# Kernel tuning notes

Measured on AMD Instinct MI355X. Metric: run time of the kernel, lower is better.

## Reference

```python
import jax, jax.numpy as jnp
import numpy as np

D, H, DH, FF, E, DHID, V, NL = 768, 12, 64, 3072, 8, 2048, 50258, 6
CAP, THRESH = 256, 0.2  # capacity = int(512 * 2.0 * 2 / 8), threshold_eval


def _ln(x, g, b):
    m = jnp.mean(x, -1, keepdims=True)
    v = jnp.mean(jnp.square(x - m), -1, keepdims=True)
    return (x - m) * jax.lax.rsqrt(v + 1e-5) * g + b


def _rms(x, g):
    return x * jax.lax.rsqrt(jnp.mean(jnp.square(x), -1, keepdims=True) + 1e-6) * g


def _attn(x, wqkv, bqkv, wo, bo):
    b, s, _ = x.shape
    q, k, v = jnp.split(x @ wqkv + bqkv, 3, axis=-1)
    q, k, v = (t.reshape(b, s, H, DH).transpose(0, 2, 1, 3) for t in (q, k, v))
    sc = jnp.einsum('bhqd,bhkd->bhqk', q, k) / 8.0  # sqrt(DH) = 8
    causal = jnp.tril(jnp.ones((s, s), bool))
    p = jax.nn.softmax(jnp.where(causal, sc, -1e9), axis=-1)
    o = jnp.einsum('bhqk,bhkd->bhqd', p, v).transpose(0, 2, 1, 3).reshape(b, s, D)
    return o @ wo + bo


def _mlp(x, w1, b1, w2, b2):  # GPT2 gelu_new = tanh approx
    return jax.nn.gelu(x @ w1 + b1, approximate=True) @ w2 + b2


def _geglu_ff(x, w1, b1, w2, b2):  # st-moe Expert FF
    a, g = jnp.split(x @ w1 + b1, 2, axis=-1)
    return (a * jax.nn.gelu(g, approximate=False)) @ w2 + b2


def _moe(x, wg, we1, be1, we2, be2):
    # top-2 gating with eval threshold + capacity-factor dispatch (ST-MoE style)
    logits = x @ wg                              # [b,s,E]
    probs = jax.nn.softmax(logits, axis=-1)
    idx1 = jnp.argmax(probs, -1)
    m1 = jax.nn.one_hot(idx1, E, dtype=x.dtype)
    gate1 = jnp.sum(probs * m1, -1)
    probs2 = probs * (1.0 - m1)
    idx2 = jnp.argmax(probs2, -1)
    m2r = jax.nn.one_hot(idx2, E, dtype=x.dtype)
    gate2 = jnp.sum(probs2 * m2r, -1)
    denom = gate1 + gate2 + 1e-9
    g1 = gate1 / denom
    keep_second = (gate2 > THRESH).astype(x.dtype)
    g2 = (gate2 / denom) * keep_second
    m2 = m2r * keep_second[..., None]
    # aux losses
    density = jnp.mean(m1, (0, 1))
    proxy = jnp.mean(probs, (0, 1))
    balance = jnp.mean(density * proxy) * (E * E)
    zloss = jnp.mean(jnp.square(jax.nn.logsumexp(logits, -1)))
    aux = 0.01 * balance + 0.001 * zloss
    # capacity positions (per batch group, first choices placed before second)
    pos1 = jnp.cumsum(m1, 1) - 1.0
    keep1 = m1 * (pos1 < CAP)
    cnt1 = jnp.sum(m1, 1, keepdims=True)
    pos2 = jnp.cumsum(m2, 1) - 1.0 + cnt1
    keep2 = m2 * (pos2 < CAP)
    oh1 = jax.nn.one_hot(pos1.astype(jnp.int32), CAP, dtype=x.dtype)
    oh2 = jax.nn.one_hot(pos2.astype(jnp.int32), CAP, dtype=x.dtype)
    combine = (g1[..., None, None] * keep1[..., None] * oh1
               + g2[..., None, None] * keep2[..., None] * oh2)  # [b,s,E,CAP]
    dispatch = (combine > 0).astype(x.dtype)
    xin = jnp.einsum('bsec,bsd->ebcd', dispatch, x)              # [E,b,CAP,D]
    h = jnp.einsum('ebcd,edf->ebcf', xin, we1) + be1[:, None, None, :]
    a, g = jnp.split(h, 2, axis=-1)
    h = a * jax.nn.gelu(g, approximate=False)
    out = jnp.einsum('ebcf,efd->ebcd', h, we2) + be2[:, None, None, :]
    y = jnp.einsum('bsec,ebcd->bsd', combine, out)
    return y, aux


def _moe_block(x, ffb_g, ffb_w1, ffb_b1, ffb_w2, ffb_b2, moe_g, w_gate,
               we1, be1, we2, be2, ffa_g, ffa_w1, ffa_b1, ffa_w2, ffa_b2):
    x = x + _geglu_ff(_rms(x, ffb_g), ffb_w1, ffb_b1, ffb_w2, ffb_b2)
    y, aux = _moe(_rms(x, moe_g), w_gate, we1, be1, we2, be2)
    x = x + y
    x = x + _geglu_ff(_rms(x, ffa_g), ffa_w1, ffa_b1, ffa_w2, ffa_b2)
    return x, aux


def _forward(input_ids, wte, wpe, ln1_g, ln1_b, w_qkv, b_qkv, w_ao, b_ao,
             ln2_g, ln2_b, w_fc, b_fc, w_mp, b_mp, lnf_g, lnf_b,
             ffb_g, ffb_w1, ffb_b1, ffb_w2, ffb_b2, moe_g, w_gate,
             we1, be1, we2, be2, ffa_g, ffa_w1, ffa_b1, ffa_w2, ffa_b2):
    s = input_ids.shape[1]
    x = wte[input_ids] + wpe[:s][None]
    aux_total = jnp.float32(0.0)
    moe_params = (ffb_g, ffb_w1, ffb_b1, ffb_w2, ffb_b2, moe_g, w_gate,
                  we1, be1, we2, be2, ffa_g, ffa_w1, ffa_b1, ffa_w2, ffa_b2)
    for i in range(NL):
        x = x + _attn(_ln(x, ln1_g[i], ln1_b[i]), w_qkv[i], b_qkv[i], w_ao[i], b_ao[i])
        h = _ln(x, ln2_g[i], ln2_b[i])
        if i in (0, 3):  # MoE layers (mlp*0 in source is a no-op)
            ff, aux = _moe_block(h, *moe_params)
            aux_total = aux_total + aux
            x = x + ff
        else:
            x = x + _mlp(h, w_fc[i], b_fc[i], w_mp[i], b_mp[i])
    x = _ln(x, lnf_g, lnf_b)
    return x @ wte.T, aux_total  # lm_head tied to wte


def setup_inputs() -> dict:
    key = jax.random.key(0)
    ks = iter(jax.random.split(key, 40))
    def nrm(shape):
        return (jax.random.normal(next(ks), shape) * 0.02).astype(jnp.float32)
    f32 = jnp.float32
    return {
        'input_ids': jax.random.randint(next(ks), (4, 512), 0, V),
        'attention_mask': jnp.ones((4, 512), jnp.int32),  # unused by the source forward
        'wte': nrm((V, D)), 'wpe': nrm((1024, D)),
        'ln1_g': jnp.ones((NL, D), f32), 'ln1_b': jnp.zeros((NL, D), f32),
        'w_qkv': nrm((NL, D, 3 * D)), 'b_qkv': jnp.zeros((NL, 3 * D), f32),
        'w_ao': nrm((NL, D, D)), 'b_ao': jnp.zeros((NL, D), f32),
        'ln2_g': jnp.ones((NL, D), f32), 'ln2_b': jnp.zeros((NL, D), f32),
        'w_fc': nrm((NL, D, FF)), 'b_fc': jnp.zeros((NL, FF), f32),
        'w_mp': nrm((NL, FF, D)), 'b_mp': jnp.zeros((NL, D), f32),
        'lnf_g': jnp.ones((D,), f32), 'lnf_b': jnp.zeros((D,), f32),
        'ffb_g': jnp.ones((D,), f32), 'ffb_w1': nrm((D, 2 * DHID)), 'ffb_b1': jnp.zeros((2 * DHID,), f32),
        'ffb_w2': nrm((DHID, D)), 'ffb_b2': jnp.zeros((D,), f32),
        'moe_g': jnp.ones((D,), f32), 'w_gate': nrm((D, E)),
        'we1': nrm((E, D, 2 * DHID)), 'be1': jnp.zeros((E, 2 * DHID), f32),
        'we2': nrm((E, DHID, D)), 'be2': jnp.zeros((E, D), f32),
        'ffa_g': jnp.ones((D,), f32), 'ffa_w1': nrm((D, 2 * DHID)), 'ffa_b1': jnp.zeros((2 * DHID,), f32),
        'ffa_w2': nrm((DHID, D)), 'ffa_b2': jnp.zeros((D,), f32),
    }


def reference(input_ids, attention_mask, wte, wpe, ln1_g, ln1_b, w_qkv, b_qkv,
              w_ao, b_ao, ln2_g, ln2_b, w_fc, b_fc, w_mp, b_mp, lnf_g, lnf_b,
              ffb_g, ffb_w1, ffb_b1, ffb_w2, ffb_b2, moe_g, w_gate,
              we1, be1, we2, be2, ffa_g, ffa_w1, ffa_b1, ffa_w2, ffa_b2):
    del attention_mask  # computed but never used in the source forward
    return _forward(input_ids, wte, wpe, ln1_g, ln1_b, w_qkv, b_qkv, w_ao, b_ao,
                    ln2_g, ln2_b, w_fc, b_fc, w_mp, b_mp, lnf_g, lnf_b,
                    ffb_g, ffb_w1, ffb_b1, ffb_w2, ffb_b2, moe_g, w_gate,
                    we1, be1, we2, be2, ffa_g, ffa_w1, ffa_b1, ffa_w2, ffa_b2)
```

## Files before the change

### kernel.cpp

```cpp
#include <hip/hip_runtime.h>
#include <math.h>

#define B_ 4
#define S_ 512
#define T_ 2048
#define D_ 768
#define H_ 12
#define DH_ 64
#define FF_ 3072
#define G_ 4096
#define DHID_ 2048
#define E_ 8
#define CAP_ 256
#define V_ 50258
#define NL_ 6

__device__ __forceinline__ float gelu_tanh_f(float x) {
    float x3 = x * x * x;
    return 0.5f * x * (1.0f + tanhf(0.7978845608028654f * (x + 0.044715f * x3)));
}
__device__ __forceinline__ float gelu_exact_f(float x) {
    return 0.5f * x * (1.0f + erff(x * 0.7071067811865475f));
}

__global__ __launch_bounds__(256) void embed_kernel(
    const int* __restrict__ ids, const float* __restrict__ wte,
    const float* __restrict__ wpe, float* __restrict__ x) {
    int t = blockIdx.x;
    int id = ids[t];
    int s = t & (S_ - 1);
    const float* wt = wte + (long long)id * D_;
    const float* wp = wpe + (long long)s * D_;
    float* o = x + (long long)t * D_;
    for (int c = threadIdx.x; c < D_; c += 256) o[c] = wt[c] + wp[c];
}

__global__ __launch_bounds__(256) void ln_kernel(
    const float* __restrict__ X, const float* __restrict__ g,
    const float* __restrict__ bb, float* __restrict__ out) {
    __shared__ float red[256];
    int t = blockIdx.x, tid = threadIdx.x;
    const float* x = X + (long long)t * D_;
    float v0 = x[tid], v1 = x[tid + 256], v2 = x[tid + 512];
    red[tid] = v0 + v1 + v2;
    __syncthreads();
    for (int o = 128; o; o >>= 1) { if (tid < o) red[tid] += red[tid + o]; __syncthreads(); }
    float mean = red[0] * (1.0f / D_);
    __syncthreads();
    float d0 = v0 - mean, d1 = v1 - mean, d2 = v2 - mean;
    red[tid] = d0 * d0 + d1 * d1 + d2 * d2;
    __syncthreads();
    for (int o = 128; o; o >>= 1) { if (tid < o) red[tid] += red[tid + o]; __syncthreads(); }
    float r = rsqrtf(red[0] * (1.0f / D_) + 1e-5f);
    float* op = out + (long long)t * D_;
    op[tid]       = d0 * r * g[tid]       + bb[tid];
    op[tid + 256] = d1 * r * g[tid + 256] + bb[tid + 256];
    op[tid + 512] = d2 * r * g[tid + 512] + bb[tid + 512];
}

__global__ __launch_bounds__(256) void rms_kernel(
    const float* __restrict__ X, const float* __restrict__ g, float* __restrict__ out) {
    __shared__ float red[256];
    int t = blockIdx.x, tid = threadIdx.x;
    const float* x = X + (long long)t * D_;
    float v0 = x[tid], v1 = x[tid + 256], v2 = x[tid + 512];
    red[tid] = v0 * v0 + v1 * v1 + v2 * v2;
    __syncthreads();
    for (int o = 128; o; o >>= 1) { if (tid < o) red[tid] += red[tid + o]; __syncthreads(); }
    float r = rsqrtf(red[0] * (1.0f / D_) + 1e-6f);
    float* op = out + (long long)t * D_;
    op[tid]       = v0 * r * g[tid];
    op[tid + 256] = v1 * r * g[tid + 256];
    op[tid + 512] = v2 * r * g[tid + 512];
}

template <int ACT, bool BIAS, bool RESID, bool BT>
__global__ __launch_bounds__(256) void gemm_kernel(
    const float* __restrict__ A, int lda, long long sA,
    const float* __restrict__ Bm, int ldb, long long sB,
    const float* __restrict__ bias, long long sBias,
    const float* __restrict__ Res,
    float* __restrict__ C, int ldc, long long sC,
    int M, int N, int K) {
    const int bz = blockIdx.z;
    const float* Ap = A + (long long)bz * sA;
    const float* Bp = Bm + (long long)bz * sB;
    const float* biasp = BIAS ? bias + (long long)bz * sBias : nullptr;
    const float* Resp = RESID ? Res + (long long)bz * sC : nullptr;
    float* Cp = C + (long long)bz * sC;

    const int m0 = blockIdx.y * 64;
    const int n0 = blockIdx.x * 64;
    const int tid = threadIdx.x;
    const int tx = tid & 15, ty = tid >> 4;

    __shared__ float As[16][65];
    __shared__ float Bs[16][65];

    float acc[4][4] = {};

    for (int k0 = 0; k0 < K; k0 += 16) {
        {
            int m = tid >> 2, kg = (tid & 3) * 4;
            float4 av = *(const float4*)(Ap + (long long)(m0 + m) * lda + k0 + kg);
            As[kg + 0][m] = av.x; As[kg + 1][m] = av.y;
            As[kg + 2][m] = av.z; As[kg + 3][m] = av.w;
        }
        if (!BT) {
            int k = tid >> 4, ng = (tid & 15) * 4;
            float4 bv = *(const float4*)(Bp + (long long)(k0 + k) * ldb + n0 + ng);
            Bs[k][ng + 0] = bv.x; Bs[k][ng + 1] = bv.y;
            Bs[k][ng + 2] = bv.z; Bs[k][ng + 3] = bv.w;
        } else {
            int n = tid >> 2, kg = (tid & 3) * 4;
            float4 bv = make_float4(0.f, 0.f, 0.f, 0.f);
            if (n0 + n < N)
                bv = *(const float4*)(Bp + (long long)(n0 + n) * ldb + k0 + kg);
            Bs[kg + 0][n] = bv.x; Bs[kg + 1][n] = bv.y;
            Bs[kg + 2][n] = bv.z; Bs[kg + 3][n] = bv.w;
        }
        __syncthreads();
#pragma unroll
        for (int k = 0; k < 16; ++k) {
            float a[4], b[4];
#pragma unroll
            for (int j = 0; j < 4; ++j) a[j] = As[k][ty * 4 + j];
#pragma unroll
            for (int j = 0; j < 4; ++j) b[j] = Bs[k][tx * 4 + j];
#pragma unroll
            for (int i = 0; i < 4; ++i)
#pragma unroll
                for (int j = 0; j < 4; ++j) acc[i][j] += a[i] * b[j];
        }
        __syncthreads();
    }

#pragma unroll
    for (int i = 0; i < 4; ++i) {
        int m = m0 + ty * 4 + i;
#pragma unroll
        for (int j = 0; j < 4; ++j) {
            int n = n0 + tx * 4 + j;
            if (n < N) {
                float v = acc[i][j];
                if (BIAS) v += biasp[n];
                if (ACT == 1) v = gelu_tanh_f(v);
                if (RESID) v += Resp[(long long)m * ldc + n];
                Cp[(long long)m * ldc + n] = v;
            }
        }
    }
}

template <int ACT, bool BIAS, bool RESID, bool BT>
static void launch_gemm(hipStream_t st, const float* A, int lda, long long sA,
                        const float* Bm, int ldb, long long sB,
                        const float* bias, long long sBias, const float* Res,
                        float* C, int ldc, long long sC, int M, int N, int K, int Z) {
    dim3 g((N + 63) / 64, M / 64, Z);
    gemm_kernel<ACT, BIAS, RESID, BT><<<g, 256, 0, st>>>(
        A, lda, sA, Bm, ldb, sB, bias, sBias, Res, C, ldc, sC, M, N, K);
}

__global__ __launch_bounds__(256) void attn_scores_kernel(
    const float* __restrict__ qkv, float* __restrict__ P) {
    int q = blockIdx.x, h = blockIdx.y, b = blockIdx.z;
    int tid = threadIdx.x;
    __shared__ float4 qv[16];
    __shared__ float red[256];
    const float* qrow = qkv + ((long long)(b * S_ + q)) * (3 * D_) + h * DH_;
    if (tid < 16) qv[tid] = *(const float4*)(qrow + tid * 4);
    __syncthreads();
    float sc[2];
#pragma unroll
    for (int r = 0; r < 2; ++r) {
        int k = tid + r * 256;
        float s = -1e30f;
        if (k <= q) {
            const float* krow = qkv + ((long long)(b * S_ + k)) * (3 * D_) + D_ + h * DH_;
            float dot = 0.f;
#pragma unroll
            for (int i = 0; i < 16; ++i) {
                float4 kv = *(const float4*)(krow + i * 4);
                float4 qq = qv[i];
                dot += qq.x * kv.x + qq.y * kv.y + qq.z * kv.z + qq.w * kv.w;
            }
            s = dot * 0.125f;
        }
        sc[r] = s;
    }
    float mx = fmaxf(sc[0], sc[1]);
    red[tid] = mx; __syncthreads();
    for (int o = 128; o; o >>= 1) { if (tid < o) red[tid] = fmaxf(red[tid], red[tid + o]); __syncthreads(); }
    mx = red[0]; __syncthreads();
    float e0 = (sc[0] > -1e29f) ? expf(sc[0] - mx) : 0.f;
    float e1 = (sc[1] > -1e29f) ? expf(sc[1] - mx) : 0.f;
    red[tid] = e0 + e1; __syncthreads();
    for (int o = 128; o; o >>= 1) { if (tid < o) red[tid] += red[tid + o]; __syncthreads(); }
    float inv = 1.0f / red[0];
    float* pr = P + (((long long)(b * H_ + h) * S_) + q) * S_;
    pr[tid] = e0 * inv;
    pr[tid + 256] = e1 * inv;
}

__global__ __launch_bounds__(64) void attn_pv_kernel(
    const float* __restrict__ qkv, const float* __restrict__ P, float* __restrict__ O) {
    int q = blockIdx.x, h = blockIdx.y, b = blockIdx.z;
    int d = threadIdx.x;
    const float* pr = P + (((long long)(b * H_ + h) * S_) + q) * S_;
    const float* vb = qkv + (long long)b * S_ * (3 * D_) + 2 * D_ + h * DH_ + d;
    float acc = 0.f;
    for (int k = 0; k <= q; ++k) acc += pr[k] * vb[(long long)k * (3 * D_)];
    O[((long long)(b * S_ + q)) * D_ + h * DH_ + d] = acc;
}

__global__ __launch_bounds__(256) void glu_kernel(
    const float* __restrict__ hb, float* __restrict__ ob, long long rows) {
    long long i = (long long)blockIdx.x * 256 + threadIdx.x;
    long long r = i >> 11;
    int c = (int)(i & (DHID_ - 1));
    float a = hb[r * G_ + c];
    float g = hb[r * G_ + DHID_ + c];
    ob[i] = a * gelu_exact_f(g);
}

__global__ __launch_bounds__(256) void moe_gate_kernel(
    const float* __restrict__ t0, const float* __restrict__ wg,
    int* __restrict__ idx1, int* __restrict__ idx2,
    float* __restrict__ g1o, float* __restrict__ g2o, float* __restrict__ red) {
    __shared__ float sred[17];
    int tid = threadIdx.x;
    if (tid < 17) sred[tid] = 0.f;
    __syncthreads();
    int t = blockIdx.x * 256 + tid;
    const float* xr = t0 + (long long)t * D_;
    float lg[E_];
#pragma unroll
    for (int e = 0; e < E_; ++e) lg[e] = 0.f;
    for (int i = 0; i < D_; ++i) {
        float xv = xr[i];
        const float* w = wg + i * E_;
#pragma unroll
        for (int e = 0; e < E_; ++e) lg[e] += xv * w[e];
    }
    float mx = lg[0];
#pragma unroll
    for (int e = 1; e < E_; ++e) mx = fmaxf(mx, lg[e]);
    float pe[E_], sum = 0.f;
#pragma unroll
    for (int e = 0; e < E_; ++e) { pe[e] = expf(lg[e] - mx); sum += pe[e]; }
    float lse = mx + logf(sum);
    float inv = 1.0f / sum;
#pragma unroll
    for (int e = 0; e < E_; ++e) pe[e] *= inv;
    int i1 = 0; float p1 = pe[0];
#pragma unroll
    for (int e = 1; e < E_; ++e) if (pe[e] > p1) { p1 = pe[e]; i1 = e; }
    int i2 = 0; float p2 = -1.f;
#pragma unroll
    for (int e = 0; e < E_; ++e) if (e != i1 && pe[e] > p2) { p2 = pe[e]; i2 = e; }
    float denom = p1 + p2 + 1e-9f;
    float g1 = p1 / denom;
    float keep = (p2 > 0.2f) ? 1.f : 0.f;
    float g2 = (p2 / denom) * keep;
    idx1[t] = i1; idx2[t] = i2; g1o[t] = g1; g2o[t] = g2;
    atomicAdd(&sred[i1], 1.0f);
#pragma unroll
    for (int e = 0; e < E_; ++e) atomicAdd(&sred[8 + e], pe[e]);
    atomicAdd(&sred[16], lse * lse);
    __syncthreads();
    if (tid < 17) atomicAdd(&red[tid], sred[tid]);
}

__global__ void aux_finalize_kernel(const float* __restrict__ red, float* __restrict__ aux) {
    if (threadIdx.x == 0 && blockIdx.x == 0) {
        float bal = 0.f;
        for (int e = 0; e < E_; ++e) bal += (red[e] / (float)T_) * (red[8 + e] / (float)T_);
        bal *= 8.f;
        float z = red[16] / (float)T_;
        aux[0] += 0.01f * bal + 0.001f * z;
    }
}

__global__ __launch_bounds__(64) void moe_scan_kernel(
    const int* __restrict__ idx1, const int* __restrict__ idx2, const float* __restrict__ g2,
    int* __restrict__ c1p, int* __restrict__ c2p, int* __restrict__ slot) {
    __shared__ int s1[T_];
    __shared__ int s2[T_];
    __shared__ unsigned char sk[T_];
    int tid = threadIdx.x;
    for (int i = tid; i < T_; i += 64) {
        s1[i] = idx1[i]; s2[i] = idx2[i]; sk[i] = (g2[i] > 0.f) ? 1 : 0;
    }
    __syncthreads();
    if (tid < 32) {
        int b = tid >> 3, e = tid & 7;
        int base = b * S_;
        int cnt = 0;
        for (int s = 0; s < S_; ++s) {
            int t = base + s;
            if (s1[t] == e) {
                int p = cnt++;
                if (p < CAP_) { c1p[t] = p; slot[(e * B_ + b) * CAP_ + p] = t; }
                else c1p[t] = -1;
            }
        }
        int cnt2 = cnt;
        for (int s = 0; s < S_; ++s) {
            int t = base + s;
            if (s2[t] == e) {
                if (sk[t]) {
                    int p = cnt2++;
                    if (p < CAP_) { c2p[t] = p; slot[(e * B_ + b) * CAP_ + p] = t; }
                    else c2p[t] = -1;
                } else c2p[t] = -1;
            }
        }
    }
}

__global__ __launch_bounds__(256) void moe_gather_kernel(
    const float* __restrict__ t0, const int* __restrict__ slot, float* __restrict__ xin) {
    int sidx = blockIdx.x;
    int tok = slot[sidx];
    float* o = xin + (long long)sidx * D_;
    if (tok >= 0) {
        const float* src = t0 + (long long)tok * D_;
        for (int c = threadIdx.x; c < D_; c += 256) o[c] = src[c];
    } else {
        for (int c = threadIdx.x; c < D_; c += 256) o[c] = 0.f;
    }
}

__global__ __launch_bounds__(256) void moe_combine_kernel(
    const float* __restrict__ eout, const int* __restrict__ idx1, const int* __restrict__ idx2,
    const int* __restrict__ c1p, const int* __restrict__ c2p,
    const float* __restrict__ g1, const float* __restrict__ g2, float* __restrict__ x1) {
    int t = blockIdx.x;
    int b = t >> 9;
    int i1 = idx1[t], i2 = idx2[t], c1 = c1p[t], c2 = c2p[t];
    float w1 = g1[t], w2 = g2[t];
    const float* r1 = (c1 >= 0) ? eout + ((long long)(i1 * B_ + b) * CAP_ + c1) * D_ : nullptr;
    const float* r2 = (c2 >= 0 && w2 > 0.f) ? eout + ((long long)(i2 * B_ + b) * CAP_ + c2) * D_ : nullptr;
    float* xr = x1 + (long long)t * D_;
    for (int c = threadIdx.x; c < D_; c += 256) {
        float y = 0.f;
        if (r1) y += w1 * r1[c];
        if (r2) y += w2 * r2[c];
        xr[c] += y;
    }
}

__global__ __launch_bounds__(256) void add_kernel(
    float* __restrict__ a, const float* __restrict__ b, int n) {
    int i = blockIdx.x * 256 + threadIdx.x;
    if (i < n) a[i] += b[i];
}

__global__ void write_aux_kernel(float* __restrict__ dst, const float* __restrict__ aux) {
    if (threadIdx.x == 0) dst[0] = aux[0];
}

extern "C" void kernel_launch(void* const* d_in, const int* in_sizes, int n_in,
                              void* d_out, int out_size, void* d_ws, size_t ws_size,
                              hipStream_t stream) {
    (void)in_sizes; (void)n_in; (void)out_size; (void)ws_size;
    const int*   ids    = (const int*)d_in[0];
    const float* wte    = (const float*)d_in[2];
    const float* wpe    = (const float*)d_in[3];
    const float* ln1_g  = (const float*)d_in[4];
    const float* ln1_b  = (const float*)d_in[5];
    const float* w_qkv  = (const float*)d_in[6];
    const float* b_qkv  = (const float*)d_in[7];
    const float* w_ao   = (const float*)d_in[8];
    const float* b_ao   = (const float*)d_in[9];
    const float* ln2_g  = (const float*)d_in[10];
    const float* ln2_b  = (const float*)d_in[11];
    const float* w_fc   = (const float*)d_in[12];
    const float* b_fc   = (const float*)d_in[13];
    const float* w_mp   = (const float*)d_in[14];
    const float* b_mp   = (const float*)d_in[15];
    const float* lnf_g  = (const float*)d_in[16];
    const float* lnf_b  = (const float*)d_in[17];
    const float* ffb_g  = (const float*)d_in[18];
    const float* ffb_w1 = (const float*)d_in[19];
    const float* ffb_b1 = (const float*)d_in[20];
    const float* ffb_w2 = (const float*)d_in[21];
    const float* ffb_b2 = (const float*)d_in[22];
    const float* moe_g  = (const float*)d_in[23];
    const float* w_gate = (const float*)d_in[24];
    const float* we1    = (const float*)d_in[25];
    const float* be1    = (const float*)d_in[26];
    const float* we2    = (const float*)d_in[27];
    const float* be2    = (const float*)d_in[28];
    const float* ffa_g  = (const float*)d_in[29];
    const float* ffa_w1 = (const float*)d_in[30];
    const float* ffa_b1 = (const float*)d_in[31];
    const float* ffa_w2 = (const float*)d_in[32];
    const float* ffa_b2 = (const float*)d_in[33];

    float* out = (float*)d_out;

    float* xf   = (float*)d_ws;
    float* aux  = xf + (long long)T_ * D_;
    float* red  = aux + 4;
    int*   idx1 = (int*)(red + 32);
    int*   idx2 = idx1 + T_;
    int*   c1p  = idx2 + T_;
    int*   c2p  = c1p + T_;
    float* g1v  = (float*)(c2p + T_);
    float* g2v  = g1v + T_;
    int*   slot = (int*)(g2v + T_);

    float* x    = out;
    float* h    = x    + (long long)T_ * D_;
    float* qkv  = h    + (long long)T_ * D_;
    float* P    = qkv  + (long long)T_ * 3 * D_;
    float* ao   = P    + (long long)B_ * H_ * S_ * S_;
    float* ffh  = ao   + (long long)T_ * D_;
    float* ffg  = ffh  + (long long)T_ * G_;
    float* x1   = ffg  + (long long)T_ * DHID_;
    float* t0   = x1   + (long long)T_ * D_;
    float* xin  = t0   + (long long)T_ * D_;
    float* eh   = xin  + (long long)E_ * B_ * CAP_ * D_;
    float* eg   = eh   + (long long)E_ * B_ * CAP_ * G_;
    float* eout = eg   + (long long)E_ * B_ * CAP_ * DHID_;

    hipMemsetAsync(aux, 0, 4, stream);

    embed_kernel<<<T_, 256, 0, stream>>>(ids, wte, wpe, x);

    for (int L = 0; L < NL_; ++L) {
        ln_kernel<<<T_, 256, 0, stream>>>(x, ln1_g + L * D_, ln1_b + L * D_, h);
        launch_gemm<0, true, false, false>(stream, h, D_, 0,
            w_qkv + (long long)L * D_ * 3 * D_, 3 * D_, 0,
            b_qkv + (long long)L * 3 * D_, 0, nullptr,
            qkv, 3 * D_, 0, T_, 3 * D_, D_, 1);
        attn_scores_kernel<<<dim3(S_, H_, B_), 256, 0, stream>>>(qkv, P);
        attn_pv_kernel<<<dim3(S_, H_, B_), 64, 0, stream>>>(qkv, P, ao);
        launch_gemm<0, true, true, false>(stream, ao, D_, 0,
            w_ao + (long long)L * D_ * D_, D_, 0,
            b_ao + (long long)L * D_, 0, x,
            x, D_, 0, T_, D_, D_, 1);

        ln_kernel<<<T_, 256, 0, stream>>>(x, ln2_g + L * D_, ln2_b + L * D_, h);

        if (L == 0 || L == 3) {
            rms_kernel<<<T_, 256, 0, stream>>>(h, ffb_g, t0);
            launch_gemm<0, true, false, false>(stream, t0, D_, 0, ffb_w1, G_, 0,
                ffb_b1, 0, nullptr, ffh, G_, 0, T_, G_, D_, 1);
            glu_kernel<<<(T_ * DHID_) / 256, 256, 0, stream>>>(ffh, ffg, T_);
            launch_gemm<0, true, true, false>(stream, ffg, DHID_, 0, ffb_w2, D_, 0,
                ffb_b2, 0, h, x1, D_, 0, T_, D_, DHID_, 1);
            rms_kernel<<<T_, 256, 0, stream>>>(x1, moe_g, t0);
            hipMemsetAsync(red, 0, 17 * sizeof(float), stream);
            moe_gate_kernel<<<T_ / 256, 256, 0, stream>>>(t0, w_gate, idx1, idx2, g1v, g2v, red);
            aux_finalize_kernel<<<1, 1, 0, stream>>>(red, aux);
            hipMemsetAsync(slot, 0xFF, E_ * B_ * CAP_ * sizeof(int), stream);
            moe_scan_kernel<<<1, 64, 0, stream>>>(idx1, idx2, g2v, c1p, c2p, slot);
            moe_gather_kernel<<<E_ * B_ * CAP_, 256, 0, stream>>>(t0, slot, xin);
            launch_gemm<0, true, false, false>(stream,
                xin, D_, (long long)B_ * CAP_ * D_,
                we1, G_, (long long)D_ * G_,
                be1, G_, nullptr,
                eh, G_, (long long)B_ * CAP_ * G_, B_ * CAP_, G_, D_, E_);
            glu_kernel<<<(E_ * B_ * CAP_ * DHID_) / 256, 256, 0, stream>>>(eh, eg, E_ * B_ * CAP_);
            launch_gemm<0, true, false, false>(stream,
                eg, DHID_, (long long)B_ * CAP_ * DHID_,
                we2, D_, (long long)DHID_ * D_,
                be2, D_, nullptr,
                eout, D_, (long long)B_ * CAP_ * D_, B_ * CAP_, D_, DHID_, E_);
            moe_combine_kernel<<<T_, 256, 0, stream>>>(eout, idx1, idx2, c1p, c2p, g1v, g2v, x1);
            add_kernel<<<(T_ * D_) / 256, 256, 0, stream>>>(x, x1, T_ * D_);
            rms_kernel<<<T_, 256, 0, stream>>>(x1, ffa_g, t0);
            launch_gemm<0, true, false, false>(stream, t0, D_, 0, ffa_w1, G_, 0,
                ffa_b1, 0, nullptr, ffh, G_, 0, T_, G_, D_, 1);
            glu_kernel<<<(T_ * DHID_) / 256, 256, 0, stream>>>(ffh, ffg, T_);
            launch_gemm<0, true, true, false>(stream, ffg, DHID_, 0, ffa_w2, D_, 0,
                ffa_b2, 0, x, x, D_, 0, T_, D_, DHID_, 1);
        } else {
            launch_gemm<1, true, false, false>(stream, h, D_, 0,
                w_fc + (long long)L * D_ * FF_, FF_, 0,
                b_fc + (long long)L * FF_, 0, nullptr,
                ffh, FF_, 0, T_, FF_, D_, 1);
            launch_gemm<0, true, true, false>(stream, ffh, FF_, 0,
                w_mp + (long long)L * FF_ * D_, D_, 0,
                b_mp + (long long)L * D_, 0, x,
                x, D_, 0, T_, D_, FF_, 1);
        }
    }

    ln_kernel<<<T_, 256, 0, stream>>>(x, lnf_g, lnf_b, xf);
    launch_gemm<0, false, false, true>(stream, xf, D_, 0, wte, D_, 0,
        nullptr, 0, nullptr, out, V_, 0, T_, V_, D_, 1);
    write_aux_kernel<<<1, 1, 0, stream>>>(out + (long long)T_ * V_, aux);
}
```

Baseline: 15.58 ms.

## Enlarge GEMM block tile to 128x128 with 8x8 per-thread register tiles

Raises the fp32 GEMM block tile from 64x64 to 128x128 while keeping 256 threads, so each thread now accumulates an 8x8 block instead of 4x4. Shared-memory reads are vectorised to float4, and the non-transposed B tile is stored to shared memory with float4 writes. The goal is more FLOPs per shared and global load and so less bandwidth-bound inner loops. The cost is higher register pressure and fewer blocks for small GEMMs, and M must now be a multiple of 128.

```diff
diff --git a/kernel.cpp b/kernel.cpp
--- a/kernel.cpp
+++ b/kernel.cpp
@@ -89,58 +89,69 @@
     const float* Resp = RESID ? Res + (long long)bz * sC : nullptr;
     float* Cp = C + (long long)bz * sC;
 
-    const int m0 = blockIdx.y * 64;
-    const int n0 = blockIdx.x * 64;
+    const int m0 = blockIdx.y * 128;
+    const int n0 = blockIdx.x * 128;
     const int tid = threadIdx.x;
     const int tx = tid & 15, ty = tid >> 4;
 
-    __shared__ float As[16][65];
-    __shared__ float Bs[16][65];
-
-    float acc[4][4] = {};
+    __shared__ float As[16][132];
+    __shared__ float Bs[16][132];
+
+    float acc[8][8] = {};
+
+    const int amr = tid >> 2;
+    const int akg = (tid & 3) * 4;
+    const int bkr = tid >> 5;
+    const int bnc = (tid & 31) * 4;
 
     for (int k0 = 0; k0 < K; k0 += 16) {
         {
-            int m = tid >> 2, kg = (tid & 3) * 4;
-            float4 av = *(const float4*)(Ap + (long long)(m0 + m) * lda + k0 + kg);
-            As[kg + 0][m] = av.x; As[kg + 1][m] = av.y;
-            As[kg + 2][m] = av.z; As[kg + 3][m] = av.w;
+            const float* Ab = Ap + (long long)(m0 + amr) * lda + k0 + akg;
+            float4 a0 = *(const float4*)Ab;
+            float4 a1 = *(const float4*)(Ab + (long long)64 * lda);
+            As[akg + 0][amr] = a0.x; As[akg + 1][amr] = a0.y;
+            As[akg + 2][amr] = a0.z; As[akg + 3][amr] = a0.w;
+            As[akg + 0][amr + 64] = a1.x; As[akg + 1][amr + 64] = a1.y;
+            As[akg + 2][amr + 64] = a1.z; As[akg + 3][amr + 64] = a1.w;
         }
         if (!BT) {
-            int k = tid >> 4, ng = (tid & 15) * 4;
-            float4 bv = *(const float4*)(Bp + (long long)(k0 + k) * ldb + n0 + ng);
-            Bs[k][ng + 0] = bv.x; Bs[k][ng + 1] = bv.y;
-            Bs[k][ng + 2] = bv.z; Bs[k][ng + 3] = bv.w;
+            const float* Bb = Bp + (long long)(k0 + bkr) * ldb + n0 + bnc;
+            *(float4*)&Bs[bkr][bnc]     = *(const float4*)Bb;
+            *(float4*)&Bs[bkr + 8][bnc] = *(const float4*)(Bb + (long long)8 * ldb);
         } else {
-            int n = tid >> 2, kg = (tid & 3) * 4;
-            float4 bv = make_float4(0.f, 0.f, 0.f, 0.f);
-            if (n0 + n < N)
-                bv = *(const float4*)(Bp + (long long)(n0 + n) * ldb + k0 + kg);
-            Bs[kg + 0][n] = bv.x; Bs[kg + 1][n] = bv.y;
-            Bs[kg + 2][n] = bv.z; Bs[kg + 3][n] = bv.w;
+            float4 b0 = make_float4(0.f, 0.f, 0.f, 0.f), b1 = b0;
+            if (n0 + amr < N)
+                b0 = *(const float4*)(Bp + (long long)(n0 + amr) * ldb + k0 + akg);
+            if (n0 + amr + 64 < N)
+                b1 = *(const float4*)(Bp + (long long)(n0 + amr + 64) * ldb + k0 + akg);
+            Bs[akg + 0][amr] = b0.x; Bs[akg + 1][amr] = b0.y;
+            Bs[akg + 2][amr] = b0.z; Bs[akg + 3][amr] = b0.w;
+            Bs[akg + 0][amr + 64] = b1.x; Bs[akg + 1][amr + 64] = b1.y;
+            Bs[akg + 2][amr + 64] = b1.z; Bs[akg + 3][amr + 64] = b1.w;
         }
         __syncthreads();
 #pragma unroll
         for (int k = 0; k < 16; ++k) {
-            float a[4], b[4];
-#pragma unroll
-            for (int j = 0; j < 4; ++j) a[j] = As[k][ty * 4 + j];
-#pragma unroll
-            for (int j = 0; j < 4; ++j) b[j] = Bs[k][tx * 4 + j];
-#pragma unroll
-            for (int i = 0; i < 4; ++i)
-#pragma unroll
-                for (int j = 0; j < 4; ++j) acc[i][j] += a[i] * b[j];
+            float4 a0 = *(const float4*)&As[k][ty * 4];
+            float4 a1 = *(const float4*)&As[k][64 + ty * 4];
+            float4 b0 = *(const float4*)&Bs[k][tx * 4];
+            float4 b1 = *(const float4*)&Bs[k][64 + tx * 4];
+            float av[8] = {a0.x, a0.y, a0.z, a0.w, a1.x, a1.y, a1.z, a1.w};
+            float bv[8] = {b0.x, b0.y, b0.z, b0.w, b1.x, b1.y, b1.z, b1.w};
+#pragma unroll
+            for (int i = 0; i < 8; ++i)
+#pragma unroll
+                for (int j = 0; j < 8; ++j) acc[i][j] += av[i] * bv[j];
         }
         __syncthreads();
     }
 
 #pragma unroll
-    for (int i = 0; i < 4; ++i) {
-        int m = m0 + ty * 4 + i;
-#pragma unroll
-        for (int j = 0; j < 4; ++j) {
-            int n = n0 + tx * 4 + j;
+    for (int i = 0; i < 8; ++i) {
+        int m = m0 + ((i & 4) ? 64 : 0) + ty * 4 + (i & 3);
+#pragma unroll
+        for (int j = 0; j < 8; ++j) {
+            int n = n0 + ((j & 4) ? 64 : 0) + tx * 4 + (j & 3);
             if (n < N) {
                 float v = acc[i][j];
                 if (BIAS) v += biasp[n];
@@ -157,7 +168,7 @@
                         const float* Bm, int ldb, long long sB,
                         const float* bias, long long sBias, const float* Res,
                         float* C, int ldc, long long sC, int M, int N, int K, int Z) {
-    dim3 g((N + 63) / 64, M / 64, Z);
+    dim3 g((N + 127) / 128, M / 128, Z);
     gemm_kernel<ACT, BIAS, RESID, BT><<<g, 256, 0, st>>>(
         A, lda, sA, Bm, ldb, sB, bias, sBias, Res, C, ldc, sC, M, N, K);
 }
```

New measurement: 13.71 ms. 12.0% less time.
